# Performance work log

Hardware: AMD Instinct MI355X
Metric: run time of the kernel (lower is better)

The kernel has to match this reference:

```python
import jax, jax.numpy as jnp
import numpy as np

VOCAB = 1_000_000
TOTAL = 819_200
BATCH = 16_384
DIM = 16


def setup_inputs() -> dict:
    key = jax.random.key(0)
    k1, k2, k3, k4 = jax.random.split(key, 4)
    feature_ids = jax.random.randint(k1, (TOTAL,), 0, VOCAB, dtype=jnp.int64 if jax.config.jax_enable_x64 else jnp.int32)
    feature_ratings = jax.random.uniform(k2, (TOTAL,), dtype=jnp.float32)
    segment_ids = jnp.sort(jax.random.randint(k3, (TOTAL,), 0, BATCH))
    weight = jax.random.normal(k4, (VOCAB, DIM), dtype=jnp.float32)
    bias = jnp.zeros((DIM,), dtype=jnp.float32)
    return {
        "feature_ids": feature_ids,
        "feature_ratings": feature_ratings,
        "segment_ids": segment_ids,
        "batch_size": BATCH,
        "weight": weight,
        "bias": bias,
    }


def reference(feature_ids, feature_ratings, segment_ids, batch_size, weight, bias):
    # gather rows [total, D], weight by per-token rating, ragged segment sum
    rows = weight[feature_ids] * feature_ratings[:, None]
    summed = jax.ops.segment_sum(rows, segment_ids, num_segments=batch_size,
                                 indices_are_sorted=True)
    return summed + bias  # [batch, D]
```

## Files before the change

### kernel.cpp

```cpp
#include <hip/hip_runtime.h>

#define DIM 16
#define K_TOK 16

__global__ void init_out_kernel(float4* __restrict__ out4,
                                const float* __restrict__ bias,
                                int n4) {
    int i = blockIdx.x * blockDim.x + threadIdx.x;
    if (i < n4) {
        int d = (i & 3) * 4;
        out4[i] = make_float4(bias[d], bias[d + 1], bias[d + 2], bias[d + 3]);
    }
}

__global__ __launch_bounds__(256) void features_linear_kernel(
    const int*   __restrict__ ids,
    const float* __restrict__ ratings,
    const int*   __restrict__ segs,
    const float* __restrict__ weight,
    float*       __restrict__ out,
    int total) {
    int tid = blockIdx.x * blockDim.x + threadIdx.x;
    int d = tid & (DIM - 1);
    int stream_id = tid >> 4;
    int t0 = stream_id * K_TOK;
    if (t0 >= total) return;

    float acc = 0.0f;
    int prev = segs[t0];

    if (t0 + K_TOK <= total) {
        const int4*   idv = (const int4*)(ids + t0);
        const float4* rv  = (const float4*)(ratings + t0);
        const int4*   sv  = (const int4*)(segs + t0);

        int4   id0 = idv[0], id1 = idv[1], id2 = idv[2], id3 = idv[3];
        float4 r0  = rv[0],  r1  = rv[1],  r2  = rv[2],  r3  = rv[3];
        int4   s0  = sv[0],  s1  = sv[1],  s2  = sv[2],  s3  = sv[3];

        float w0  = weight[(size_t)id0.x * DIM + d];
        float w1  = weight[(size_t)id0.y * DIM + d];
        float w2  = weight[(size_t)id0.z * DIM + d];
        float w3  = weight[(size_t)id0.w * DIM + d];
        float w4  = weight[(size_t)id1.x * DIM + d];
        float w5  = weight[(size_t)id1.y * DIM + d];
        float w6  = weight[(size_t)id1.z * DIM + d];
        float w7  = weight[(size_t)id1.w * DIM + d];
        float w8  = weight[(size_t)id2.x * DIM + d];
        float w9  = weight[(size_t)id2.y * DIM + d];
        float w10 = weight[(size_t)id2.z * DIM + d];
        float w11 = weight[(size_t)id2.w * DIM + d];
        float w12 = weight[(size_t)id3.x * DIM + d];
        float w13 = weight[(size_t)id3.y * DIM + d];
        float w14 = weight[(size_t)id3.z * DIM + d];
        float w15 = weight[(size_t)id3.w * DIM + d];

        #define STEP(sv_, wv_, rv_)                                        \
            if ((sv_) != prev) {                                           \
                atomicAdd(&out[prev * DIM + d], acc);                      \
                acc = 0.0f; prev = (sv_);                                  \
            }                                                              \
            acc = fmaf((wv_), (rv_), acc);

        STEP(s0.x, w0,  r0.x)  STEP(s0.y, w1,  r0.y)
        STEP(s0.z, w2,  r0.z)  STEP(s0.w, w3,  r0.w)
        STEP(s1.x, w4,  r1.x)  STEP(s1.y, w5,  r1.y)
        STEP(s1.z, w6,  r1.z)  STEP(s1.w, w7,  r1.w)
        STEP(s2.x, w8,  r2.x)  STEP(s2.y, w9,  r2.y)
        STEP(s2.z, w10, r2.z)  STEP(s2.w, w11, r2.w)
        STEP(s3.x, w12, r3.x)  STEP(s3.y, w13, r3.y)
        STEP(s3.z, w14, r3.z)  STEP(s3.w, w15, r3.w)
        #undef STEP
    } else {
        for (int t = t0; t < total; ++t) {
            int seg = segs[t];
            if (seg != prev) {
                atomicAdd(&out[prev * DIM + d], acc);
                acc = 0.0f;
                prev = seg;
            }
            acc = fmaf(weight[(size_t)ids[t] * DIM + d], ratings[t], acc);
        }
    }
    atomicAdd(&out[prev * DIM + d], acc);
}

extern "C" void kernel_launch(void* const* d_in, const int* in_sizes, int n_in,
                              void* d_out, int out_size, void* d_ws, size_t ws_size,
                              hipStream_t stream) {
    const int*   ids     = (const int*)d_in[0];
    const float* ratings = (const float*)d_in[1];
    const int*   segs    = (const int*)d_in[2];
    const float* weight  = (const float*)d_in[4];
    const float* bias    = (const float*)d_in[5];
    float* out = (float*)d_out;

    int total = in_sizes[0];

    {
        int n4 = out_size / 4;
        int threads = 256;
        int blocks = (n4 + threads - 1) / threads;
        init_out_kernel<<<blocks, threads, 0, stream>>>((float4*)out, bias, n4);
    }

    {
        int n_streams = (total + K_TOK - 1) / K_TOK;
        long long n_threads = (long long)n_streams * DIM;
        int threads = 256;
        int blocks = (int)((n_threads + threads - 1) / threads);
        features_linear_kernel<<<blocks, threads, 0, stream>>>(
            ids, ratings, segs, weight, out, total);
    }
}
```

Measured before the change: 116.5 us.

## Assign one segment per thread group via binary search, drop atomics and init kernel

Replaces the token-parallel kernel, which flushed partial sums with atomicAdd, with a segment-parallel kernel. Each group of 16 lanes binary-searches the sorted segment ids for its segment's token range and accumulates the gathered weighted rows. It then writes the output plus bias directly, which removes the separate init kernel and all atomics. In exchange it adds a roughly 20-step dependent binary search per thread and loses parallelism: 16384 segments give only 262k threads, and segment lengths vary, so load is uneven.

```diff
diff --git a/kernel.cpp b/kernel.cpp
--- a/kernel.cpp
+++ b/kernel.cpp
@@ -1,88 +1,63 @@
 #include <hip/hip_runtime.h>
 
 #define DIM 16
-#define K_TOK 16
 
-__global__ void init_out_kernel(float4* __restrict__ out4,
-                                const float* __restrict__ bias,
-                                int n4) {
-    int i = blockIdx.x * blockDim.x + threadIdx.x;
-    if (i < n4) {
-        int d = (i & 3) * 4;
-        out4[i] = make_float4(bias[d], bias[d + 1], bias[d + 2], bias[d + 3]);
-    }
-}
-
-__global__ __launch_bounds__(256) void features_linear_kernel(
+__global__ __launch_bounds__(256) void features_linear_seg_kernel(
     const int*   __restrict__ ids,
     const float* __restrict__ ratings,
     const int*   __restrict__ segs,
     const float* __restrict__ weight,
+    const float* __restrict__ bias,
     float*       __restrict__ out,
-    int total) {
+    int total,
+    int batch) {
     int tid = blockIdx.x * blockDim.x + threadIdx.x;
     int d = tid & (DIM - 1);
-    int stream_id = tid >> 4;
-    int t0 = stream_id * K_TOK;
-    if (t0 >= total) return;
+    int b = tid >> 4;
+    if (b >= batch) return;
 
+    int lo0 = 0, n0 = total;
+    int lo1 = 0, n1 = total;
+    int last = total - 1;
+    while ((n0 | n1) != 0) {
+        int h0 = n0 >> 1; int m0 = lo0 + h0; m0 = m0 < last ? m0 : last;
+        int h1 = n1 >> 1; int m1 = lo1 + h1; m1 = m1 < last ? m1 : last;
+        int v0 = segs[m0];
+        int v1 = segs[m1];
+        bool p0 = (n0 > 0) & (v0 < b);
+        bool p1 = (n1 > 0) & (v1 <= b);
+        lo0 = p0 ? m0 + 1 : lo0;
+        lo1 = p1 ? m1 + 1 : lo1;
+        n0  = p0 ? (n0 - h0 - 1) : h0;
+        n1  = p1 ? (n1 - h1 - 1) : h1;
+    }
+
+    const char* wb = (const char*)weight;
+    unsigned db = (unsigned)d << 2;
     float acc = 0.0f;
-    int prev = segs[t0];
 
-    if (t0 + K_TOK <= total) {
-        const int4*   idv = (const int4*)(ids + t0);
-        const float4* rv  = (const float4*)(ratings + t0);
-        const int4*   sv  = (const int4*)(segs + t0);
+    int lastt = lo1 - 1;
+    for (int base = lo0; base < lo1; base += 16) {
+        int   idv[16];
+        float rv[16];
+        #pragma unroll
+        for (int i = 0; i < 16; ++i) {
+            int t  = base + i;
+            int tc = t < lastt ? t : lastt;
+            idv[i] = ids[tc];
+            float r = ratings[tc];
+            rv[i]  = (t <= lastt) ? r : 0.0f;
+        }
+        float wv[16];
+        #pragma unroll
+        for (int i = 0; i < 16; ++i)
+            wv[i] = *(const float*)(wb + (((unsigned)idv[i]) << 6) + db);
+        #pragma unroll
+        for (int i = 0; i < 16; ++i)
+            acc = fmaf(wv[i], rv[i], acc);
+    }
 
-        int4   id0 = idv[0], id1 = idv[1], id2 = idv[2], id3 = idv[3];
-        float4 r0  = rv[0],  r1  = rv[1],  r2  = rv[2],  r3  = rv[3];
-        int4   s0  = sv[0],  s1  = sv[1],  s2  = sv[2],  s3  = sv[3];
-
-        float w0  = weight[(size_t)id0.x * DIM + d];
-        float w1  = weight[(size_t)id0.y * DIM + d];
-        float w2  = weight[(size_t)id0.z * DIM + d];
-        float w3  = weight[(size_t)id0.w * DIM + d];
-        float w4  = weight[(size_t)id1.x * DIM + d];
-        float w5  = weight[(size_t)id1.y * DIM + d];
-        float w6  = weight[(size_t)id1.z * DIM + d];
-        float w7  = weight[(size_t)id1.w * DIM + d];
-        float w8  = weight[(size_t)id2.x * DIM + d];
-        float w9  = weight[(size_t)id2.y * DIM + d];
-        float w10 = weight[(size_t)id2.z * DIM + d];
-        float w11 = weight[(size_t)id2.w * DIM + d];
-        float w12 = weight[(size_t)id3.x * DIM + d];
-        float w13 = weight[(size_t)id3.y * DIM + d];
-        float w14 = weight[(size_t)id3.z * DIM + d];
-        float w15 = weight[(size_t)id3.w * DIM + d];
-
-        #define STEP(sv_, wv_, rv_)                                        \
-            if ((sv_) != prev) {                                           \
-                atomicAdd(&out[prev * DIM + d], acc);                      \
-                acc = 0.0f; prev = (sv_);                                  \
-            }                                                              \
-            acc = fmaf((wv_), (rv_), acc);
-
-        STEP(s0.x, w0,  r0.x)  STEP(s0.y, w1,  r0.y)
-        STEP(s0.z, w2,  r0.z)  STEP(s0.w, w3,  r0.w)
-        STEP(s1.x, w4,  r1.x)  STEP(s1.y, w5,  r1.y)
-        STEP(s1.z, w6,  r1.z)  STEP(s1.w, w7,  r1.w)
-        STEP(s2.x, w8,  r2.x)  STEP(s2.y, w9,  r2.y)
-        STEP(s2.z, w10, r2.z)  STEP(s2.w, w11, r2.w)
-        STEP(s3.x, w12, r3.x)  STEP(s3.y, w13, r3.y)
-        STEP(s3.z, w14, r3.z)  STEP(s3.w, w15, r3.w)
-        #undef STEP
-    } else {
-        for (int t = t0; t < total; ++t) {
-            int seg = segs[t];
-            if (seg != prev) {
-                atomicAdd(&out[prev * DIM + d], acc);
-                acc = 0.0f;
-                prev = seg;
-            }
-            acc = fmaf(weight[(size_t)ids[t] * DIM + d], ratings[t], acc);
-        }
-    }
-    atomicAdd(&out[prev * DIM + d], acc);
+    out[(((unsigned)b) << 4) + d] = acc + bias[d];
 }
 
 extern "C" void kernel_launch(void* const* d_in, const int* in_sizes, int n_in,
@@ -96,20 +71,11 @@
     float* out = (float*)d_out;
 
     int total = in_sizes[0];
+    int batch = out_size / DIM;
 
-    {
-        int n4 = out_size / 4;
-        int threads = 256;
-        int blocks = (n4 + threads - 1) / threads;
-        init_out_kernel<<<blocks, threads, 0, stream>>>((float4*)out, bias, n4);
-    }
-
-    {
-        int n_streams = (total + K_TOK - 1) / K_TOK;
-        long long n_threads = (long long)n_streams * DIM;
-        int threads = 256;
-        int blocks = (int)((n_threads + threads - 1) / threads);
-        features_linear_kernel<<<blocks, threads, 0, stream>>>(
-            ids, ratings, segs, weight, out, total);
-    }
+    long long n_threads = (long long)batch * DIM;
+    int threads = 256;
+    int blocks = (int)((n_threads + threads - 1) / threads);
+    features_linear_seg_kernel<<<blocks, threads, 0, stream>>>(
+        ids, ratings, segs, weight, bias, out, total, batch);
 }
```

New measurement: 119.7 us. 1.03x slower.
